# Optimization experiments

Hardware: AMD Instinct MI355X
Metric: run time of the kernel (lower is better)

The kernel has to match this reference:

```python
import jax, jax.numpy as jnp
import numpy as np

NUM_GROUPS = 4
NUM_HEADS = 4
EPS = 1e-6

def group_norm(x, scale, bias):
    # x: [B, C, L]
    b, c, l = x.shape
    g = NUM_GROUPS
    xg = x.reshape(b, g, (c // g) * l)
    mean = xg.mean(axis=-1, keepdims=True)
    var = xg.var(axis=-1, keepdims=True)
    xg = (xg - mean) * jax.lax.rsqrt(var + EPS)
    xn = xg.reshape(b, c, l)
    return xn * scale[None, :, None] + bias[None, :, None]

def conv1x1(x, w, b):
    # x: [B, C_in, L], w: [C_out, C_in], b: [C_out]
    return jnp.einsum('oc,bcl->bol', w, x) + b[None, :, None]

def setup_inputs() -> dict:
    key = jax.random.key(0)
    ks = jax.random.split(key, 11)
    B, C, L = 8, 512, 2048
    x = jax.random.normal(ks[0], (B, C, L), dtype=jnp.float32)
    s = 1.0 / np.sqrt(C)
    return {
        'x': x,
        'gn_scale': jnp.ones((C,), jnp.float32),
        'gn_bias': jnp.zeros((C,), jnp.float32),
        'wq': jax.random.normal(ks[1], (C, C), jnp.float32) * s,
        'bq': jnp.zeros((C,), jnp.float32),
        'wk': jax.random.normal(ks[2], (C, C), jnp.float32) * s,
        'bk': jnp.zeros((C,), jnp.float32),
        'wv': jax.random.normal(ks[3], (C, C), jnp.float32) * s,
        'bv': jnp.zeros((C,), jnp.float32),
        'wo': jax.random.normal(ks[4], (C, C), jnp.float32) * s,
        'bo': jnp.zeros((C,), jnp.float32),
    }

def reference(x, gn_scale, gn_bias, wq, bq, wk, bk, wv, bv, wo, bo):
    b, c, l = x.shape
    nh = NUM_HEADS
    hd = c // nh
    h_ = group_norm(x, gn_scale, gn_bias)
    q = conv1x1(h_, wq, bq).reshape(b, nh, hd, l)
    k = conv1x1(h_, wk, bk).reshape(b, nh, hd, l)
    v = conv1x1(h_, wv, bv).reshape(b, nh, hd, l)
    # scores: [b, nh, l(query), l(key)]
    w_ = jnp.einsum('bhdq,bhdk->bhqk', q, k) * (hd ** -0.5)
    w_ = jax.nn.softmax(w_, axis=-1)
    # attn: [b, nh, l(query), hd]
    attn = jnp.einsum('bhqk,bhdk->bhqd', w_, v)
    attn = attn.transpose(0, 1, 3, 2).reshape(b, c, l)
    out = conv1x1(attn, wo, bo)
    return x + out
```

## Files before the change

kernel.cpp:

```cpp
#include <hip/hip_runtime.h>


typedef unsigned short u16;
typedef unsigned long long u64;
typedef __attribute__((ext_vector_type(8)))  short          bf16x8;
typedef __attribute__((ext_vector_type(4)))  float          f32x4;
typedef __attribute__((ext_vector_type(4)))  unsigned int   u32x4;
typedef __attribute__((ext_vector_type(8)))  unsigned short u16x8;

#define MFMA16(a, b, c) __builtin_amdgcn_mfma_f32_16x16x32_bf16((a), (b), (c), 0, 0, 0)

__device__ __forceinline__ u16 f2bf(float f) {
    union { float f; unsigned int i; } cv;
    cv.f = f;
    unsigned int u = cv.i;
    u += 0x7fffu + ((u >> 16) & 1);
    return (u16)(u >> 16);
}

__device__ __forceinline__ void async16(const u16* g, u16* l) {
    __builtin_amdgcn_global_load_lds(
        (const __attribute__((address_space(1))) unsigned int*)g,
        (__attribute__((address_space(3))) unsigned int*)l, 16, 0, 0);
}

#define BATCH 8
#define CCH   512
#define LEN   2048
#define NGRP  4
#define NHEAD 4
#define HD    128
#define GSIZE (128 * 2048)

__global__ __launch_bounds__(256) void wcvt_k(const float* __restrict__ w0,
                                              const float* __restrict__ w1,
                                              const float* __restrict__ w2,
                                              const float* __restrict__ w3,
                                              u16* __restrict__ dst) {
    const int mat = blockIdx.y;
    const float* src = (mat == 0) ? w0 : (mat == 1) ? w1 : (mat == 2) ? w2 : w3;
    const size_t base = (size_t)blockIdx.x * 2048 + (size_t)threadIdx.x * 8;
    f32x4 a = *(const f32x4*)(src + base);
    f32x4 b = *(const f32x4*)(src + base + 4);
    u16x8 o;
    for (int u = 0; u < 4; ++u) { o[u] = f2bf(a[u]); o[u + 4] = f2bf(b[u]); }
    *(u16x8*)(dst + (size_t)mat * 262144 + base) = o;
}

__global__ __launch_bounds__(256) void gn_stats_k(const float* __restrict__ x,
                                                  float* __restrict__ stats) {
    const int bid   = blockIdx.x;
    const int grp   = bid >> 3;
    const int chunk = bid & 7;
    const int b = grp >> 2, g = grp & 3;
    const float* base = x + ((size_t)(b * CCH + g * 128 + chunk * 16)) * LEN;

    float s = 0.f, ss = 0.f;
    for (int i = 0; i < 32; ++i) {
        int cid = threadIdx.x + i * 256;
        f32x4 dv = *(const f32x4*)(base + (size_t)cid * 4);
        for (int u = 0; u < 4; ++u) { s += dv[u]; ss += dv[u] * dv[u]; }
    }
    for (int m = 1; m < 64; m <<= 1) {
        s  += __shfl_xor(s,  m, 64);
        ss += __shfl_xor(ss, m, 64);
    }
    __shared__ float red[8];
    int wid = threadIdx.x >> 6, lane = threadIdx.x & 63;
    if (lane == 0) { red[wid * 2] = s; red[wid * 2 + 1] = ss; }
    __syncthreads();
    if (threadIdx.x == 0) {
        float ts  = red[0] + red[2] + red[4] + red[6];
        float tss = red[1] + red[3] + red[5] + red[7];
        atomicAdd(&stats[grp * 2],     ts);
        atomicAdd(&stats[grp * 2 + 1], tss);
    }
}

__global__ __launch_bounds__(256) void gn_apply_k(const float* __restrict__ x,
                                                  const float* __restrict__ gns,
                                                  const float* __restrict__ gnb,
                                                  const float* __restrict__ stats,
                                                  u16* __restrict__ hT) {
    __shared__ u16 Ts[64 * 72];
    const int b = blockIdx.z, c0 = blockIdx.y * 64, l0 = blockIdx.x * 64;
    const int g = c0 >> 7;
    const int tid = threadIdx.x;

    float sum   = stats[(b * NGRP + g) * 2];
    float sumsq = stats[(b * NGRP + g) * 2 + 1];
    const float invN = 1.f / (float)GSIZE;
    float mean = sum * invN;
    float var  = sumsq * invN - mean * mean;
    float rstd = rsqrtf(var + 1e-6f);

    for (int i = 0; i < 4; ++i) {
        int cid = tid + i * 256;
        int row = cid >> 4, c4 = cid & 15;
        int c = c0 + row;
        float sc = gns[c] * rstd;
        float bi = gnb[c] - mean * sc;
        f32x4 dv = *(const f32x4*)(x + ((size_t)(b * CCH + c)) * LEN + l0 + c4 * 4);
        for (int u = 0; u < 4; ++u)
            Ts[row * 72 + c4 * 4 + u] = f2bf(dv[u] * sc + bi);
    }
    __syncthreads();
    for (int i = 0; i < 2; ++i) {
        int cid = tid + i * 256;
        int lrow = cid >> 3, c8 = cid & 7;
        u16x8 ov;
        for (int u = 0; u < 8; ++u) ov[u] = Ts[(c8 * 8 + u) * 72 + lrow];
        *(u16x8*)(hT + ((size_t)b * LEN + l0 + lrow) * CCH + c0 + c8 * 8) = ov;
    }
}

template <int MODE>
__global__ __launch_bounds__(256, 2) void gemm_k(const u16* __restrict__ A0,
                                                 const u16* __restrict__ B0,
                                                 const u16* __restrict__ B1,
                                                 const float* __restrict__ bias0,
                                                 const float* __restrict__ bias1,
                                                 const float* __restrict__ resid,
                                                 void* __restrict__ out0v,
                                                 u16* __restrict__ out1) {
    __shared__ u16 As[128 * 64];
    __shared__ u16 Bs[128 * 64];
    const int b  = blockIdx.z;
    const int n0 = blockIdx.x * 128;
    const int m0 = blockIdx.y * 128;
    const int tid = threadIdx.x;
    const int lane = tid & 63, wid = tid >> 6;
    const int quad = lane >> 4, l15 = lane & 15;
    const int wm = (wid & 1) * 64, wn = (wid >> 1) * 64;

    const u16* Arow;
    if constexpr (MODE == 0) Arow = A0 + ((size_t)b * LEN + m0) * 512;
    else                     Arow = A0 + (size_t)m0 * 512;

    const u16* Brow;
    int col0 = 0;
    if constexpr (MODE == 0) {
        if (n0 < 512) { Brow = B0 + (size_t)n0 * 512;         col0 = n0; }
        else          { Brow = B1 + (size_t)(n0 - 512) * 512;  col0 = n0 - 512; }
    } else {
        Brow = B0 + ((size_t)b * LEN + n0) * 512;
    }

    f32x4 acc[4][4] = {};
    const int srl = lane >> 3, scl = lane & 7;

    for (int kk = 0; kk < 8; ++kk) {
        const int k0 = kk * 64;
        __syncthreads();
#pragma unroll
        for (int i = 0; i < 4; ++i) {
            int rloc = wid * 32 + i * 8 + srl;
            int lc = scl ^ (rloc & 7);
            async16(Arow + (size_t)rloc * 512 + k0 + lc * 8, &As[(wid * 32 + i * 8) * 64]);
            async16(Brow + (size_t)rloc * 512 + k0 + lc * 8, &Bs[(wid * 32 + i * 8) * 64]);
        }
        __syncthreads();
        for (int ks = 0; ks < 2; ++ks) {
            bf16x8 af[4], bfr[4];
            for (int t = 0; t < 4; ++t) {
                int ra = wm + t * 16 + l15, rb = wn + t * 16 + l15;
                af[t]  = *(const bf16x8*)(&As[ra * 64 + (((ks * 4 + quad) ^ (ra & 7))) * 8]);
                bfr[t] = *(const bf16x8*)(&Bs[rb * 64 + (((ks * 4 + quad) ^ (rb & 7))) * 8]);
            }
            for (int mt = 0; mt < 4; ++mt)
                for (int nt = 0; nt < 4; ++nt)
                    acc[mt][nt] = MFMA16(af[mt], bfr[nt], acc[mt][nt]);
        }
    }

    if constexpr (MODE == 0) {
        const float* biasp = (n0 < 512) ? (bias0 + col0) : (bias1 + col0);
        u16* outp = (n0 < 512) ? (u16*)out0v : out1;
        for (int nt = 0; nt < 4; ++nt) {
            int nl = wn + nt * 16 + l15;
            float bv_ = biasp[nl];
            for (int mt = 0; mt < 4; ++mt)
                for (int r = 0; r < 4; ++r) {
                    int ml = wm + mt * 16 + quad * 4 + r;
                    size_t idx = ((size_t)b * LEN + m0 + ml) * 512 + col0 + nl;
                    outp[idx] = f2bf(acc[mt][nt][r] + bv_);
                }
        }
    } else {
        for (int mt = 0; mt < 4; ++mt)
            for (int r = 0; r < 4; ++r) {
                int ml = wm + mt * 16 + quad * 4 + r;
                float bv_ = bias0[m0 + ml];
                for (int nt = 0; nt < 4; ++nt) {
                    int nl = wn + nt * 16 + l15;
                    size_t idx = ((size_t)(b * 512 + m0 + ml)) * LEN + n0 + nl;
                    float val = acc[mt][nt][r] + bv_;
                    if constexpr (MODE == 2) {
                        ((float*)out0v)[idx] = val + resid[idx];
                    } else {
                        ((u16*)out0v)[idx] = f2bf(val);
                    }
                }
            }
    }
}

__global__ __launch_bounds__(256, 2) void attn_k(const u16* __restrict__ qT,
                                                 const u16* __restrict__ kT,
                                                 const u16* __restrict__ v,
                                                 u16* __restrict__ attnT) {
    __shared__ u16 Ks[128 * 128];
    __shared__ u16 Vs[128 * 128];
    const int b = blockIdx.z, h = blockIdx.y;
    const int i0 = blockIdx.x * 128;
    const int tid = threadIdx.x, lane = tid & 63, wid = tid >> 6;
    const int quad = lane >> 4, l15 = lane & 15;

    bf16x8 qa[2][4];
    for (int mf = 0; mf < 2; ++mf)
        for (int ks = 0; ks < 4; ++ks) {
            int m = i0 + wid * 32 + mf * 16 + l15;
            qa[mf][ks] = *(const bf16x8*)(qT + ((size_t)b * LEN + m) * 512 + h * HD +
                                          ks * 32 + quad * 8);
        }

    float mst[2] = {-3.0e38f, -3.0e38f}, lst[2] = {0.f, 0.f};
    f32x4 oacc[2][8] = {};

    const float SL2E = 0.08838834764831845f * 1.4426950408889634f;

    const int srw = lane >> 4, sc = lane & 15;
    const u16* kbase = kT + ((size_t)b * LEN) * 512 + h * HD;
    const u16* vbase = v + ((size_t)(b * CCH + h * HD)) * LEN;

    for (int jt = 0; jt < 16; ++jt) {
        const int j0 = jt * 128;
        __syncthreads();
#pragma unroll
        for (int i = 0; i < 8; ++i) {
            int rloc = wid * 32 + i * 4 + srw;
            int lc = sc ^ (rloc & 7);
            async16(kbase + (size_t)(j0 + rloc) * 512 + lc * 8,
                    &Ks[(wid * 32 + i * 4) * 128]);
            async16(vbase + (size_t)rloc * LEN + j0 + lc * 8,
                    &Vs[(wid * 32 + i * 4) * 128]);
        }
        __syncthreads();

        f32x4 st[2][8] = {};
        for (int nt = 0; nt < 8; ++nt) {
            int r = nt * 16 + l15;
            for (int ks = 0; ks < 4; ++ks) {
                bf16x8 kf = *(const bf16x8*)(&Ks[r * 128 + ((ks * 4 + quad) ^ (r & 7)) * 8]);
                st[0][nt] = MFMA16(kf, qa[0][ks], st[0][nt]);
                st[1][nt] = MFMA16(kf, qa[1][ks], st[1][nt]);
            }
        }

        for (int mf = 0; mf < 2; ++mf) {
            float rm = -3.0e38f;
            for (int nt = 0; nt < 8; ++nt)
                for (int r = 0; r < 4; ++r) rm = fmaxf(rm, st[mf][nt][r]);
            rm *= SL2E;
            rm = fmaxf(rm, __shfl_xor(rm, 16, 64));
            rm = fmaxf(rm, __shfl_xor(rm, 32, 64));
            float mnew  = fmaxf(mst[mf], rm);
            float alpha = __builtin_amdgcn_exp2f(mst[mf] - mnew);
            mst[mf] = mnew;
            float rs = 0.f;
            for (int nt = 0; nt < 8; ++nt)
                for (int r = 0; r < 4; ++r) {
                    float p = __builtin_amdgcn_exp2f(st[mf][nt][r] * SL2E - mnew);
                    st[mf][nt][r] = p;
                    rs += p;
                }
            rs += __shfl_xor(rs, 16, 64);
            rs += __shfl_xor(rs, 32, 64);
            lst[mf] = lst[mf] * alpha + rs;
            float av[4];
            for (int r = 0; r < 4; ++r) av[r] = __shfl(alpha, quad * 4 + r, 16);
            for (int dt = 0; dt < 8; ++dt)
                for (int r = 0; r < 4; ++r) oacc[mf][dt][r] *= av[r];
        }

        __syncthreads();

        for (int mf = 0; mf < 2; ++mf) {
            int m = wid * 32 + mf * 16 + l15;
            for (int nt = 0; nt < 8; ++nt) {
                u64 packed =  (u64)f2bf(st[mf][nt][0])
                           | ((u64)f2bf(st[mf][nt][1]) << 16)
                           | ((u64)f2bf(st[mf][nt][2]) << 32)
                           | ((u64)f2bf(st[mf][nt][3]) << 48);
                int pc = (nt * 2 + (quad >> 1)) ^ (m & 7);
                *(u64*)(&Ks[m * 128 + pc * 8 + (quad & 1) * 4]) = packed;
            }
        }

        for (int ks = 0; ks < 4; ++ks) {
            bf16x8 pf[2];
            for (int mf = 0; mf < 2; ++mf) {
                int m = wid * 32 + mf * 16 + l15;
                pf[mf] = *(const bf16x8*)(&Ks[m * 128 + ((ks * 4 + quad) ^ (m & 7)) * 8]);
            }
            for (int dt = 0; dt < 8; ++dt) {
                int d = dt * 16 + l15;
                bf16x8 vf = *(const bf16x8*)(&Vs[d * 128 + ((ks * 4 + quad) ^ (d & 7)) * 8]);
                oacc[0][dt] = MFMA16(pf[0], vf, oacc[0][dt]);
                oacc[1][dt] = MFMA16(pf[1], vf, oacc[1][dt]);
            }
        }
    }

    for (int mf = 0; mf < 2; ++mf) {
        float inv = 1.f / lst[mf];
        float iv[4];
        for (int r = 0; r < 4; ++r) iv[r] = __shfl(inv, quad * 4 + r, 16);
        for (int r = 0; r < 4; ++r) {
            int m = i0 + wid * 32 + mf * 16 + quad * 4 + r;
            for (int dt = 0; dt < 8; ++dt) {
                int d = dt * 16 + l15;
                attnT[((size_t)b * LEN + m) * 512 + h * HD + d] =
                    f2bf(oacc[mf][dt][r] * iv[r]);
            }
        }
    }
}

extern "C" void kernel_launch(void* const* d_in, const int* in_sizes, int n_in,
                              void* d_out, int out_size, void* d_ws, size_t ws_size,
                              hipStream_t stream) {
    const float* x   = (const float*)d_in[0];
    const float* gns = (const float*)d_in[1];
    const float* gnb = (const float*)d_in[2];
    const float* wq  = (const float*)d_in[3];
    const float* bq  = (const float*)d_in[4];
    const float* wk  = (const float*)d_in[5];
    const float* bk  = (const float*)d_in[6];
    const float* wv  = (const float*)d_in[7];
    const float* bv  = (const float*)d_in[8];
    const float* wo  = (const float*)d_in[9];
    const float* bo  = (const float*)d_in[10];
    float* out = (float*)d_out;

    const size_t NEL = (size_t)BATCH * CCH * LEN;
    float* stats = (float*)d_ws;
    u16* wcat  = (u16*)((char*)d_ws + 256);
    u16* hT    = wcat + 4 * 262144;
    u16* qT    = hT + NEL;
    u16* kT    = qT + NEL;
    u16* vbuf  = kT + NEL;
    u16* attnT = hT;

    const u16* wq_bf = wcat;
    const u16* wk_bf = wcat + 262144;
    const u16* wv_bf = wcat + 2 * 262144;
    const u16* wo_bf = wcat + 3 * 262144;

    hipMemsetAsync(d_ws, 0, 256, stream);
    wcvt_k<<<dim3(128, 4), 256, 0, stream>>>(wq, wk, wv, wo, wcat);
    gn_stats_k<<<256, 256, 0, stream>>>(x, stats);
    gn_apply_k<<<dim3(32, 8, 8), 256, 0, stream>>>(x, gns, gnb, stats, hT);
    gemm_k<0><<<dim3(8, 16, 8), 256, 0, stream>>>(hT, wq_bf, wk_bf, bq, bk, nullptr, qT, kT);
    gemm_k<1><<<dim3(16, 4, 8), 256, 0, stream>>>(wv_bf, hT, nullptr, bv, nullptr, nullptr, vbuf, nullptr);
    attn_k<<<dim3(16, 4, 8), 256, 0, stream>>>(qT, kT, vbuf, attnT);
    gemm_k<2><<<dim3(16, 4, 8), 256, 0, stream>>>(wo_bf, attnT, nullptr, bo, nullptr, x, out, nullptr);
}
```

Measured before the change: 290.1 us.

## Double-buffer LDS tiles in GEMM and attention, prefetching next tile asynchronously

```diff
diff --git a/kernel.cpp b/kernel.cpp
--- a/kernel.cpp
+++ b/kernel.cpp
@@ -2,6 +2,7 @@
 
 
 typedef unsigned short u16;
+typedef unsigned int   u32;
 typedef unsigned long long u64;
 typedef __attribute__((ext_vector_type(8)))  short          bf16x8;
 typedef __attribute__((ext_vector_type(4)))  float          f32x4;
@@ -16,6 +17,9 @@
     unsigned int u = cv.i;
     u += 0x7fffu + ((u >> 16) & 1);
     return (u16)(u >> 16);
+}
+__device__ __forceinline__ u32 fbits(float f) {
+    union { float f; unsigned int i; } cv; cv.f = f; return cv.i;
 }
 
 __device__ __forceinline__ void async16(const u16* g, u16* l) {
@@ -123,8 +127,8 @@
                                                  const float* __restrict__ resid,
                                                  void* __restrict__ out0v,
                                                  u16* __restrict__ out1) {
-    __shared__ u16 As[128 * 64];
-    __shared__ u16 Bs[128 * 64];
+    __shared__ u16 As[2][128 * 64];
+    __shared__ u16 Bs[2][128 * 64];
     const int b  = blockIdx.z;
     const int n0 = blockIdx.x * 128;
     const int m0 = blockIdx.y * 128;
@@ -149,28 +153,42 @@
     f32x4 acc[4][4] = {};
     const int srl = lane >> 3, scl = lane & 7;
 
+#pragma unroll
+    for (int i = 0; i < 4; ++i) {
+        int rloc = wid * 32 + i * 8 + srl;
+        int lc = scl ^ (rloc & 7);
+        async16(Arow + (size_t)rloc * 512 + lc * 8, &As[0][(wid * 32 + i * 8) * 64]);
+        async16(Brow + (size_t)rloc * 512 + lc * 8, &Bs[0][(wid * 32 + i * 8) * 64]);
+    }
+    __syncthreads();
+
     for (int kk = 0; kk < 8; ++kk) {
-        const int k0 = kk * 64;
-        __syncthreads();
-#pragma unroll
-        for (int i = 0; i < 4; ++i) {
-            int rloc = wid * 32 + i * 8 + srl;
-            int lc = scl ^ (rloc & 7);
-            async16(Arow + (size_t)rloc * 512 + k0 + lc * 8, &As[(wid * 32 + i * 8) * 64]);
-            async16(Brow + (size_t)rloc * 512 + k0 + lc * 8, &Bs[(wid * 32 + i * 8) * 64]);
-        }
-        __syncthreads();
+        const int p = kk & 1;
+        if (kk < 7) {
+            const int k0n = (kk + 1) * 64;
+#pragma unroll
+            for (int i = 0; i < 4; ++i) {
+                int rloc = wid * 32 + i * 8 + srl;
+                int lc = scl ^ (rloc & 7);
+                async16(Arow + (size_t)rloc * 512 + k0n + lc * 8,
+                        &As[1 - p][(wid * 32 + i * 8) * 64]);
+                async16(Brow + (size_t)rloc * 512 + k0n + lc * 8,
+                        &Bs[1 - p][(wid * 32 + i * 8) * 64]);
+            }
+        }
+#pragma unroll
         for (int ks = 0; ks < 2; ++ks) {
             bf16x8 af[4], bfr[4];
             for (int t = 0; t < 4; ++t) {
                 int ra = wm + t * 16 + l15, rb = wn + t * 16 + l15;
-                af[t]  = *(const bf16x8*)(&As[ra * 64 + (((ks * 4 + quad) ^ (ra & 7))) * 8]);
-                bfr[t] = *(const bf16x8*)(&Bs[rb * 64 + (((ks * 4 + quad) ^ (rb & 7))) * 8]);
+                af[t]  = *(const bf16x8*)(&As[p][ra * 64 + (((ks * 4 + quad) ^ (ra & 7))) * 8]);
+                bfr[t] = *(const bf16x8*)(&Bs[p][rb * 64 + (((ks * 4 + quad) ^ (rb & 7))) * 8]);
             }
             for (int mt = 0; mt < 4; ++mt)
                 for (int nt = 0; nt < 4; ++nt)
                     acc[mt][nt] = MFMA16(af[mt], bfr[nt], acc[mt][nt]);
         }
+        __syncthreads();
     }
 
     if constexpr (MODE == 0) {
@@ -209,8 +227,8 @@
                                                  const u16* __restrict__ kT,
                                                  const u16* __restrict__ v,
                                                  u16* __restrict__ attnT) {
-    __shared__ u16 Ks[128 * 128];
-    __shared__ u16 Vs[128 * 128];
+    __shared__ u16 Ks[2][64 * 128];
+    __shared__ u16 Vs[2][128 * 64];
     const int b = blockIdx.z, h = blockIdx.y;
     const int i0 = blockIdx.x * 128;
     const int tid = threadIdx.x, lane = tid & 63, wid = tid >> 6;
@@ -229,38 +247,58 @@
 
     const float SL2E = 0.08838834764831845f * 1.4426950408889634f;
 
-    const int srw = lane >> 4, sc = lane & 15;
+    const int srwK = lane >> 4, scK = lane & 15;
+    const int srwV = lane >> 3, scV = lane & 7;
     const u16* kbase = kT + ((size_t)b * LEN) * 512 + h * HD;
     const u16* vbase = v + ((size_t)(b * CCH + h * HD)) * LEN;
 
-    for (int jt = 0; jt < 16; ++jt) {
-        const int j0 = jt * 128;
-        __syncthreads();
-#pragma unroll
-        for (int i = 0; i < 8; ++i) {
-            int rloc = wid * 32 + i * 4 + srw;
-            int lc = sc ^ (rloc & 7);
-            async16(kbase + (size_t)(j0 + rloc) * 512 + lc * 8,
-                    &Ks[(wid * 32 + i * 4) * 128]);
-            async16(vbase + (size_t)rloc * LEN + j0 + lc * 8,
-                    &Vs[(wid * 32 + i * 4) * 128]);
-        }
-        __syncthreads();
-
-        f32x4 st[2][8] = {};
-        for (int nt = 0; nt < 8; ++nt) {
-            int r = nt * 16 + l15;
+#pragma unroll
+    for (int i = 0; i < 4; ++i) {
+        int rk = wid * 16 + i * 4 + srwK;
+        int lck = scK ^ (rk & 7);
+        async16(kbase + (size_t)rk * 512 + lck * 8, &Ks[0][(wid * 16 + i * 4) * 128]);
+        int rv = wid * 32 + i * 8 + srwV;
+        int lcv = scV ^ (rv & 7);
+        async16(vbase + (size_t)rv * LEN + lcv * 8, &Vs[0][(wid * 32 + i * 8) * 64]);
+    }
+    __syncthreads();
+
+    for (int jt = 0; jt < 32; ++jt) {
+        const int p = jt & 1;
+        const int j0 = jt * 64;
+
+        if (jt < 31) {
+            const int j0n = j0 + 64;
+#pragma unroll
+            for (int i = 0; i < 4; ++i) {
+                int rk = wid * 16 + i * 4 + srwK;
+                int lck = scK ^ (rk & 7);
+                async16(kbase + (size_t)(j0n + rk) * 512 + lck * 8,
+                        &Ks[1 - p][(wid * 16 + i * 4) * 128]);
+                int rv = wid * 32 + i * 8 + srwV;
+                int lcv = scV ^ (rv & 7);
+                async16(vbase + (size_t)rv * LEN + j0n + lcv * 8,
+                        &Vs[1 - p][(wid * 32 + i * 8) * 64]);
+            }
+        }
+
+        f32x4 st[2][4] = {};
+#pragma unroll
+        for (int jtn = 0; jtn < 4; ++jtn) {
+            int r = jtn * 16 + l15;
             for (int ks = 0; ks < 4; ++ks) {
-                bf16x8 kf = *(const bf16x8*)(&Ks[r * 128 + ((ks * 4 + quad) ^ (r & 7)) * 8]);
-                st[0][nt] = MFMA16(kf, qa[0][ks], st[0][nt]);
-                st[1][nt] = MFMA16(kf, qa[1][ks], st[1][nt]);
-            }
-        }
-
+                bf16x8 kf = *(const bf16x8*)(&Ks[p][r * 128 + ((ks * 4 + quad) ^ (r & 7)) * 8]);
+                st[0][jtn] = MFMA16(kf, qa[0][ks], st[0][jtn]);
+                st[1][jtn] = MFMA16(kf, qa[1][ks], st[1][jtn]);
+            }
+        }
+
+        float alpha2[2];
+#pragma unroll
         for (int mf = 0; mf < 2; ++mf) {
             float rm = -3.0e38f;
-            for (int nt = 0; nt < 8; ++nt)
-                for (int r = 0; r < 4; ++r) rm = fmaxf(rm, st[mf][nt][r]);
+            for (int jtn = 0; jtn < 4; ++jtn)
+                for (int r = 0; r < 4; ++r) rm = fmaxf(rm, st[mf][jtn][r]);
             rm *= SL2E;
             rm = fmaxf(rm, __shfl_xor(rm, 16, 64));
             rm = fmaxf(rm, __shfl_xor(rm, 32, 64));
@@ -268,48 +306,58 @@
             float alpha = __builtin_amdgcn_exp2f(mst[mf] - mnew);
             mst[mf] = mnew;
             float rs = 0.f;
-            for (int nt = 0; nt < 8; ++nt)
+            for (int jtn = 0; jtn < 4; ++jtn)
                 for (int r = 0; r < 4; ++r) {
-                    float p = __builtin_amdgcn_exp2f(st[mf][nt][r] * SL2E - mnew);
-                    st[mf][nt][r] = p;
-                    rs += p;
+                    float pv_ = __builtin_amdgcn_exp2f(st[mf][jtn][r] * SL2E - mnew);
+                    st[mf][jtn][r] = pv_;
+                    rs += pv_;
                 }
             rs += __shfl_xor(rs, 16, 64);
             rs += __shfl_xor(rs, 32, 64);
             lst[mf] = lst[mf] * alpha + rs;
-            float av[4];
-            for (int r = 0; r < 4; ++r) av[r] = __shfl(alpha, quad * 4 + r, 16);
-            for (int dt = 0; dt < 8; ++dt)
-                for (int r = 0; r < 4; ++r) oacc[mf][dt][r] *= av[r];
+            alpha2[mf] = alpha;
+        }
+        if (__ballot(alpha2[0] != 1.0f || alpha2[1] != 1.0f) != 0ull) {
+#pragma unroll
+            for (int mf = 0; mf < 2; ++mf) {
+                float av[4];
+                for (int r = 0; r < 4; ++r) av[r] = __shfl(alpha2[mf], quad * 4 + r, 16);
+                for (int dt = 0; dt < 8; ++dt)
+                    for (int r = 0; r < 4; ++r) oacc[mf][dt][r] *= av[r];
+            }
         }
 
         __syncthreads();
 
+#pragma unroll
         for (int mf = 0; mf < 2; ++mf) {
             int m = wid * 32 + mf * 16 + l15;
-            for (int nt = 0; nt < 8; ++nt) {
-                u64 packed =  (u64)f2bf(st[mf][nt][0])
-                           | ((u64)f2bf(st[mf][nt][1]) << 16)
-                           | ((u64)f2bf(st[mf][nt][2]) << 32)
-                           | ((u64)f2bf(st[mf][nt][3]) << 48);
-                int pc = (nt * 2 + (quad >> 1)) ^ (m & 7);
-                *(u64*)(&Ks[m * 128 + pc * 8 + (quad & 1) * 4]) = packed;
-            }
-        }
-
-        for (int ks = 0; ks < 4; ++ks) {
+            for (int jtn = 0; jtn < 4; ++jtn) {
+                u64 packed =  (u64)((fbits(st[mf][jtn][0]) + 0x8000u) >> 16)
+                           | ((u64)((fbits(st[mf][jtn][1]) + 0x8000u) >> 16) << 16)
+                           | ((u64)((fbits(st[mf][jtn][2]) + 0x8000u) >> 16) << 32)
+                           | ((u64)((fbits(st[mf][jtn][3]) + 0x8000u) >> 16) << 48);
+                int pc = (jtn * 2 + (quad >> 1)) ^ (m & 7);
+                *(u64*)(&Ks[p][m * 64 + pc * 8 + (quad & 1) * 4]) = packed;
+            }
+        }
+
+#pragma unroll
+        for (int ks = 0; ks < 2; ++ks) {
             bf16x8 pf[2];
             for (int mf = 0; mf < 2; ++mf) {
                 int m = wid * 32 + mf * 16 + l15;
-                pf[mf] = *(const bf16x8*)(&Ks[m * 128 + ((ks * 4 + quad) ^ (m & 7)) * 8]);
+                pf[mf] = *(const bf16x8*)(&Ks[p][m * 64 + ((ks * 4 + quad) ^ (m & 7)) * 8]);
             }
             for (int dt = 0; dt < 8; ++dt) {
                 int d = dt * 16 + l15;
-                bf16x8 vf = *(const bf16x8*)(&Vs[d * 128 + ((ks * 4 + quad) ^ (d & 7)) * 8]);
+                bf16x8 vf = *(const bf16x8*)(&Vs[p][d * 64 + ((ks * 4 + quad) ^ (d & 7)) * 8]);
                 oacc[0][dt] = MFMA16(pf[0], vf, oacc[0][dt]);
                 oacc[1][dt] = MFMA16(pf[1], vf, oacc[1][dt]);
             }
         }
+
+        __syncthreads();
     }
 
     for (int mf = 0; mf < 2; ++mf) {
```

After: 276.6 us. 1.05x faster.
